# Kernel optimization log

Hardware: AMD Instinct MI355X
Metric: run time of the kernel (lower is better)

Reference implementation:

```python
import jax, jax.numpy as jnp
import numpy as np

NEG_INF = -9e15  # matches the torch source's large-negative mask value
LRELU_SLOPE = 0.2


def setup_inputs() -> dict:
    key = jax.random.key(0)
    k1, k2, k3, k4, k5, k6 = jax.random.split(key, 6)
    N, D_IN, D_OUT = 8192, 512, 256
    h = jax.random.normal(k1, (N, D_IN), dtype=jnp.float32)
    adj = jax.random.randint(k2, (N, N), 0, 2, dtype=jnp.int32)
    # xavier_uniform with gain=1.414 for W [out, in] and a [1, 2*out]
    lim_W = 1.414 * np.sqrt(6.0 / (D_IN + D_OUT))
    lim_a = 1.414 * np.sqrt(6.0 / (2 * D_OUT + 1))
    W_w = jax.random.uniform(k3, (D_OUT, D_IN), minval=-lim_W, maxval=lim_W, dtype=jnp.float32)
    W_b = jax.random.normal(k4, (D_OUT,), dtype=jnp.float32) * 0.01
    a_w = jax.random.uniform(k5, (1, 2 * D_OUT), minval=-lim_a, maxval=lim_a, dtype=jnp.float32)
    a_b = jax.random.normal(k6, (1,), dtype=jnp.float32) * 0.01
    return {"h": h, "adj": adj, "W_w": W_w, "W_b": W_b, "a_w": a_w, "a_b": a_b}


def reference(h, adj, W_w, W_b, a_w, a_b):
    # wh = W(h): [N, d_out]
    wh = h @ W_w.T + W_b
    d_out = wh.shape[-1]
    # a(cat([wh_i, wh_j])) decomposes: a_src . wh_i + a_dst . wh_j + a_b
    # (identical math to the O(N^2 * 2d) repeat/cat in the torch source)
    a_src, a_dst = a_w[0, :d_out], a_w[0, d_out:]
    s_src = wh @ a_src  # [N]
    s_dst = wh @ a_dst  # [N]
    e = jax.nn.leaky_relu(s_src[:, None] + s_dst[None, :] + a_b[0], LRELU_SLOPE)  # [N, N]
    masked = jnp.where(adj > 0, e, jnp.float32(NEG_INF))
    attn = jax.nn.softmax(masked, axis=1)  # softmax over neighbors j
    return attn @ wh  # [N, d_out]
```

## Files before the change

### kernel.cpp

```cpp
#include <hip/hip_runtime.h>

typedef unsigned short ushort_t;
typedef unsigned int uint_t;
typedef __attribute__((ext_vector_type(8))) short short8;
typedef __attribute__((ext_vector_type(4))) float f32x4;
typedef __attribute__((ext_vector_type(4))) int i32x4;
typedef __attribute__((ext_vector_type(4))) uint_t u32x4;
typedef __attribute__((ext_vector_type(4))) ushort_t u16x4;

#define LRELU_SLOPE 0.2f

static __device__ __forceinline__ float bf2f(ushort_t h) {
    uint_t u = ((uint_t)h) << 16;
    return __builtin_bit_cast(float, u);
}
static __device__ __forceinline__ ushort_t f2bf(float f) {
    uint_t u = __builtin_bit_cast(uint_t, f);
    uint_t r = (u + 0x7fffu + ((u >> 16) & 1u)) >> 16;
    return (ushort_t)r;
}
static __device__ __forceinline__ uint4 pack8(float4 a, float4 b) {
    uint4 r;
    r.x = (uint_t)f2bf(a.x) | ((uint_t)f2bf(a.y) << 16);
    r.y = (uint_t)f2bf(a.z) | ((uint_t)f2bf(a.w) << 16);
    r.z = (uint_t)f2bf(b.x) | ((uint_t)f2bf(b.y) << 16);
    r.w = (uint_t)f2bf(b.z) | ((uint_t)f2bf(b.w) << 16);
    return r;
}

__launch_bounds__(256, 2)
__global__ void k1_gemm(const float* __restrict__ h, const float* __restrict__ W,
                        const float* __restrict__ Wb, const float* __restrict__ aw,
                        ushort_t* __restrict__ whT, float* __restrict__ s_src,
                        float* __restrict__ s_dst) {
    __shared__ __align__(16) ushort_t aT[256 * 72];
    __shared__ __align__(16) ushort_t bT[32 * 72];
    __shared__ float redLds[2][4][32];

    const int t = threadIdx.x;
    const int wv = t >> 6, ln = t & 63;
    const int i0 = blockIdx.x * 32;
    const int srow = t >> 3, sch = t & 7;
    const int row0 = ln & 15, kq = ln >> 4;

    f32x4 acc[4][2];
#pragma unroll
    for (int mt = 0; mt < 4; ++mt)
#pragma unroll
        for (int nt = 0; nt < 2; ++nt) acc[mt][nt] = (f32x4){0.f, 0.f, 0.f, 0.f};

    for (int k0 = 0; k0 < 512; k0 += 64) {
        __syncthreads();
#pragma unroll
        for (int r = 0; r < 8; ++r) {
            const float* gp = W + (size_t)(r * 32 + srow) * 512 + k0 + sch * 8;
            float4 x0 = *(const float4*)gp;
            float4 x1 = *(const float4*)(gp + 4);
            *(uint4*)(aT + (r * 32 + srow) * 72 + sch * 8) = pack8(x0, x1);
        }
        {
            const float* gp = h + (size_t)(i0 + srow) * 512 + k0 + sch * 8;
            float4 x0 = *(const float4*)gp;
            float4 x1 = *(const float4*)(gp + 4);
            *(uint4*)(bT + srow * 72 + sch * 8) = pack8(x0, x1);
        }
        __syncthreads();
#pragma unroll
        for (int ks = 0; ks < 2; ++ks) {
            short8 b[2];
#pragma unroll
            for (int nt = 0; nt < 2; ++nt)
                b[nt] = *(const short8*)(bT + (nt * 16 + row0) * 72 + ks * 32 + kq * 8);
#pragma unroll
            for (int mt = 0; mt < 4; ++mt) {
                short8 a = *(const short8*)(aT + (wv * 64 + mt * 16 + row0) * 72 + ks * 32 + kq * 8);
#pragma unroll
                for (int nt = 0; nt < 2; ++nt)
                    acc[mt][nt] = __builtin_amdgcn_mfma_f32_16x16x32_bf16(a, b[nt], acc[mt][nt], 0, 0, 0);
            }
        }
    }

    float psrc[2] = {0.f, 0.f}, pdst[2] = {0.f, 0.f};
#pragma unroll
    for (int mt = 0; mt < 4; ++mt) {
#pragma unroll
        for (int r = 0; r < 4; ++r) {
            const int o = wv * 64 + mt * 16 + (ln >> 4) * 4 + r;
            const float wbv = Wb[o];
            const float as = aw[o];
            const float ad = aw[256 + o];
#pragma unroll
            for (int nt = 0; nt < 2; ++nt) {
                const float v = acc[mt][nt][r] + wbv;
                psrc[nt] += v * as;
                pdst[nt] += v * ad;
                const int i = i0 + nt * 16 + (ln & 15);
                whT[(size_t)o * 8192 + i] = f2bf(v);
            }
        }
    }
#pragma unroll
    for (int off = 16; off < 64; off <<= 1) {
#pragma unroll
        for (int nt = 0; nt < 2; ++nt) {
            psrc[nt] += __shfl_xor(psrc[nt], off, 64);
            pdst[nt] += __shfl_xor(pdst[nt], off, 64);
        }
    }
    if (ln < 16) {
#pragma unroll
        for (int nt = 0; nt < 2; ++nt) {
            redLds[0][wv][nt * 16 + ln] = psrc[nt];
            redLds[1][wv][nt * 16 + ln] = pdst[nt];
        }
    }
    __syncthreads();
    if (t < 32) {
        float s = 0.f;
#pragma unroll
        for (int w = 0; w < 4; ++w) s += redLds[0][w][t];
        s_src[i0 + t] = s;
    } else if (t < 64) {
        float s = 0.f;
#pragma unroll
        for (int w = 0; w < 4; ++w) s += redLds[1][w][t - 32];
        s_dst[i0 + t - 32] = s;
    }
}

__launch_bounds__(512, 4)
__global__ void k2_attn(const int* __restrict__ adj, const ushort_t* __restrict__ whT,
                        const float* __restrict__ s_src, const float* __restrict__ s_dst,
                        const float* __restrict__ ab_p, float* __restrict__ out0,
                        float* __restrict__ out1, float* __restrict__ zp, int jsplit) {
    __shared__ __align__(16) ushort_t wLds[256 * 72];
    __shared__ __align__(16) ushort_t pLds[32 * 72];
    __shared__ float zLds[32];

    const int t = threadIdx.x;
    const int wv = t >> 6, ln = t & 63;
    const int dq = wv & 3, kh = wv >> 2;
    const int split2 = (jsplit == 2);
    const int jb = split2 ? (int)(blockIdx.x & 1) : 0;
    const int ib = split2 ? (int)(blockIdx.x >> 1) : (int)blockIdx.x;
    const int i0 = ib * 32;
    const int jlen = split2 ? 4096 : 8192;
    const int jbase = jb * jlen;
    const int iters = jlen >> 6;
    const int prow = t >> 4, pjc = t & 15;
    const int srow = t >> 3, sch = t & 7;

    const float ab = ab_p[0];
    const float ssrc = s_src[i0 + prow];

    const int* aBase = adj + (size_t)(i0 + prow) * 8192 + jbase + pjc * 4;
    const float* sBase = s_dst + jbase + pjc * 4;
    const ushort_t* wBase = whT + (size_t)srow * 8192 + jbase + sch * 8;
    ushort_t* pDst = pLds + prow * 72 + pjc * 4;

    f32x4 acc[2][4];
#pragma unroll
    for (int mt = 0; mt < 2; ++mt)
#pragma unroll
        for (int nt = 0; nt < 4; ++nt) acc[mt][nt] = (f32x4){0.f, 0.f, 0.f, 0.f};
    float zacc = 0.f;

    i32x4 Av = *(const i32x4*)aBase;
    f32x4 Sv = *(const f32x4*)sBase;
    u32x4 Wv[4];
#pragma unroll
    for (int r = 0; r < 4; ++r) Wv[r] = *(const u32x4*)(wBase + (size_t)r * 64 * 8192);

    for (int it = 0; it < iters; ++it) {
        const int jn = (it < iters - 1) ? (it + 1) * 64 : it * 64;
        i32x4 Ac = Av;
        f32x4 Sc = Sv;
        u32x4 Wc[4];
#pragma unroll
        for (int r = 0; r < 4; ++r) Wc[r] = Wv[r];
        Av = *(const i32x4*)(aBase + jn);
        Sv = *(const f32x4*)(sBase + jn);
#pragma unroll
        for (int r = 0; r < 4; ++r) Wv[r] = *(const u32x4*)(wBase + (size_t)r * 64 * 8192 + jn);

        __syncthreads();
#pragma unroll
        for (int r = 0; r < 4; ++r)
            *(u32x4*)(wLds + (r * 64 + srow) * 72 + sch * 8) = Wc[r];
        {
            u16x4 pv4;
            float z4 = 0.f;
#pragma unroll
            for (int k = 0; k < 4; ++k) {
                float sc = ssrc + Sc[k] + ab;
                sc = sc > 0.f ? sc : LRELU_SLOPE * sc;
                sc = fminf(sc, 60.f);
                float pv = (Ac[k] > 0) ? __expf(sc) : 0.f;
                z4 += pv;
                pv4[k] = f2bf(pv);
            }
            zacc += z4;
            *(u16x4*)pDst = pv4;
        }
        __syncthreads();
        {
            short8 b[4];
#pragma unroll
            for (int nt = 0; nt < 4; ++nt)
                b[nt] = *(const short8*)(wLds + (dq * 64 + nt * 16 + (ln & 15)) * 72 + kh * 32 + (ln >> 4) * 8);
#pragma unroll
            for (int mt = 0; mt < 2; ++mt) {
                short8 a = *(const short8*)(pLds + (mt * 16 + (ln & 15)) * 72 + kh * 32 + (ln >> 4) * 8);
#pragma unroll
                for (int nt = 0; nt < 4; ++nt)
                    acc[mt][nt] = __builtin_amdgcn_mfma_f32_16x16x32_bf16(a, b[nt], acc[mt][nt], 0, 0, 0);
            }
        }
    }

    zacc += __shfl_xor(zacc, 1, 64);
    zacc += __shfl_xor(zacc, 2, 64);
    zacc += __shfl_xor(zacc, 4, 64);
    zacc += __shfl_xor(zacc, 8, 64);
    if (split2) {
        if ((t & 15) == 0) zp[(size_t)jb * 8192 + i0 + prow] = zacc;
    } else {
        if ((t & 15) == 0) zLds[prow] = 1.0f / fmaxf(zacc, 1e-30f);
    }

    __syncthreads();
    float* ex = (float*)wLds;
    if (kh == 1) {
        float* p = ex + (dq * 64 + ln) * 33;
#pragma unroll
        for (int mt = 0; mt < 2; ++mt)
#pragma unroll
            for (int nt = 0; nt < 4; ++nt)
#pragma unroll
                for (int r = 0; r < 4; ++r) p[mt * 16 + nt * 4 + r] = acc[mt][nt][r];
    }
    __syncthreads();
    if (kh == 0) {
        float* outp = (jb == 0) ? out0 : out1;
        const float* p = ex + (dq * 64 + ln) * 33;
#pragma unroll
        for (int mt = 0; mt < 2; ++mt)
#pragma unroll
            for (int nt = 0; nt < 4; ++nt)
#pragma unroll
                for (int r = 0; r < 4; ++r) {
                    const int il = mt * 16 + (ln >> 4) * 4 + r;
                    const int d = dq * 64 + nt * 16 + (ln & 15);
                    const float v = acc[mt][nt][r] + p[mt * 16 + nt * 4 + r];
                    if (split2)
                        outp[(size_t)(i0 + il) * 256 + d] = v;
                    else
                        outp[(size_t)(i0 + il) * 256 + d] = v * zLds[il];
                }
    }
}

__global__ void k3_norm(float* __restrict__ out, const float* __restrict__ part,
                        const float* __restrict__ zp) {
    const int i = blockIdx.x, t = threadIdx.x;
    const float rz = 1.0f / fmaxf(zp[i] + zp[8192 + i], 1e-30f);
    const size_t idx = (size_t)i * 256 + t;
    out[idx] = (out[idx] + part[idx]) * rz;
}

extern "C" void kernel_launch(void* const* d_in, const int* in_sizes, int n_in, void* d_out,
                              int out_size, void* d_ws, size_t ws_size, hipStream_t stream) {
    int order[16];
    for (int i = 0; i < n_in; ++i) order[i] = i;
    for (int a = 0; a < n_in; ++a)
        for (int b = a + 1; b < n_in; ++b)
            if (in_sizes[order[b]] < in_sizes[order[a]]) {
                int tmp = order[a]; order[a] = order[b]; order[b] = tmp;
            }
    const float* ab = (const float*)d_in[order[0]];
    const float* Wb = (const float*)d_in[order[1]];
    const float* aw = (const float*)d_in[order[2]];
    const float* Ww = (const float*)d_in[order[3]];
    const float* h = (const float*)d_in[order[4]];
    const int* adj = (const int*)d_in[order[5]];

    char* ws = (char*)d_ws;
    ushort_t* whT = (ushort_t*)ws;
    float* ssrc = (float*)(ws + 4194304);
    float* sdst = (float*)(ws + 4227072);
    float* part = (float*)(ws + 4259840);
    float* zp = (float*)(ws + 12648448);
    const size_t need = 12713984;
    const int jsplit = (ws_size >= need) ? 2 : 1;

    hipLaunchKernelGGL(k1_gemm, dim3(256), dim3(256), 0, stream, h, Ww, Wb, aw, whT, ssrc, sdst);
    hipLaunchKernelGGL(k2_attn, dim3(256 * jsplit), dim3(512), 0, stream, adj, whT, ssrc, sdst,
                       ab, (float*)d_out, part, zp, jsplit);
    if (jsplit == 2)
        hipLaunchKernelGGL(k3_norm, dim3(8192), dim3(256), 0, stream, (float*)d_out, part, zp);
}
```

Measured before the change: 442.5 us.

## Pre-swizzle wh into MFMA fragment layout and load B operands directly from global

The first kernel now writes wh in a blocked layout that matches the MFMA B-fragment order. The attention kernel can then load B operands straight from global memory into registers, which removes the per-iteration LDS staging of a 256x64 tile. The P tile is double-buffered in LDS, so one of the two barriers per iteration is dropped, and adj is read with nontemporal loads. In exchange, each wave loads its own B fragments from global memory or L2 with no LDS sharing, and the whB write pattern in the first kernel becomes more scattered.

```diff
diff --git a/kernel.cpp b/kernel.cpp
--- a/kernel.cpp
+++ b/kernel.cpp
@@ -10,10 +10,6 @@
 
 #define LRELU_SLOPE 0.2f
 
-static __device__ __forceinline__ float bf2f(ushort_t h) {
-    uint_t u = ((uint_t)h) << 16;
-    return __builtin_bit_cast(float, u);
-}
 static __device__ __forceinline__ ushort_t f2bf(float f) {
     uint_t u = __builtin_bit_cast(uint_t, f);
     uint_t r = (u + 0x7fffu + ((u >> 16) & 1u)) >> 16;
@@ -31,7 +27,7 @@
 __launch_bounds__(256, 2)
 __global__ void k1_gemm(const float* __restrict__ h, const float* __restrict__ W,
                         const float* __restrict__ Wb, const float* __restrict__ aw,
-                        ushort_t* __restrict__ whT, float* __restrict__ s_src,
+                        ushort_t* __restrict__ whB, float* __restrict__ s_src,
                         float* __restrict__ s_dst) {
     __shared__ __align__(16) ushort_t aT[256 * 72];
     __shared__ __align__(16) ushort_t bT[32 * 72];
@@ -96,7 +92,10 @@
                 psrc[nt] += v * as;
                 pdst[nt] += v * ad;
                 const int i = i0 + nt * 16 + (ln & 15);
-                whT[(size_t)o * 8192 + i] = f2bf(v);
+                const int jt = i >> 6;
+                const int khi = (i >> 5) & 1;
+                const int kqi = (i >> 3) & 3;
+                whB[((size_t)(jt * 2 + khi) * 256 + o) * 32 + kqi * 8 + (i & 7)] = f2bf(v);
             }
         }
     }
@@ -130,17 +129,19 @@
 }
 
 __launch_bounds__(512, 4)
-__global__ void k2_attn(const int* __restrict__ adj, const ushort_t* __restrict__ whT,
+__global__ void k2_attn(const int* __restrict__ adj, const ushort_t* __restrict__ whB,
                         const float* __restrict__ s_src, const float* __restrict__ s_dst,
                         const float* __restrict__ ab_p, float* __restrict__ out0,
                         float* __restrict__ out1, float* __restrict__ zp, int jsplit) {
-    __shared__ __align__(16) ushort_t wLds[256 * 72];
-    __shared__ __align__(16) ushort_t pLds[32 * 72];
-    __shared__ float zLds[32];
+    __shared__ __align__(16) char smem[33792 + 128];
+    ushort_t* pbuf = (ushort_t*)smem;
+    float* exch = (float*)smem;
+    float* zLds = (float*)(smem + 33792);
 
     const int t = threadIdx.x;
     const int wv = t >> 6, ln = t & 63;
     const int dq = wv & 3, kh = wv >> 2;
+    const int row0 = ln & 15, kq = ln >> 4;
     const int split2 = (jsplit == 2);
     const int jb = split2 ? (int)(blockIdx.x & 1) : 0;
     const int ib = split2 ? (int)(blockIdx.x >> 1) : (int)blockIdx.x;
@@ -149,15 +150,14 @@
     const int jbase = jb * jlen;
     const int iters = jlen >> 6;
     const int prow = t >> 4, pjc = t & 15;
-    const int srow = t >> 3, sch = t & 7;
 
     const float ab = ab_p[0];
     const float ssrc = s_src[i0 + prow];
 
     const int* aBase = adj + (size_t)(i0 + prow) * 8192 + jbase + pjc * 4;
     const float* sBase = s_dst + jbase + pjc * 4;
-    const ushort_t* wBase = whT + (size_t)srow * 8192 + jbase + sch * 8;
-    ushort_t* pDst = pLds + prow * 72 + pjc * 4;
+    const ushort_t* bBase = whB + ((size_t)(jbase >> 6) * 2 + kh) * 8192
+                            + (dq * 64 + row0) * 32 + kq * 8;
 
     f32x4 acc[2][4];
 #pragma unroll
@@ -166,28 +166,28 @@
         for (int nt = 0; nt < 4; ++nt) acc[mt][nt] = (f32x4){0.f, 0.f, 0.f, 0.f};
     float zacc = 0.f;
 
-    i32x4 Av = *(const i32x4*)aBase;
+    i32x4 Av = __builtin_nontemporal_load((const i32x4*)aBase);
     f32x4 Sv = *(const f32x4*)sBase;
-    u32x4 Wv[4];
-#pragma unroll
-    for (int r = 0; r < 4; ++r) Wv[r] = *(const u32x4*)(wBase + (size_t)r * 64 * 8192);
+    short8 Bv[4];
+#pragma unroll
+    for (int nt = 0; nt < 4; ++nt) Bv[nt] = *(const short8*)(bBase + nt * 512);
 
     for (int it = 0; it < iters; ++it) {
-        const int jn = (it < iters - 1) ? (it + 1) * 64 : it * 64;
+        const int itn = (it < iters - 1) ? it + 1 : it;
+        const int jn = itn * 64;
         i32x4 Ac = Av;
         f32x4 Sc = Sv;
-        u32x4 Wc[4];
-#pragma unroll
-        for (int r = 0; r < 4; ++r) Wc[r] = Wv[r];
-        Av = *(const i32x4*)(aBase + jn);
+        short8 Bc[4];
+#pragma unroll
+        for (int nt = 0; nt < 4; ++nt) Bc[nt] = Bv[nt];
+        Av = __builtin_nontemporal_load((const i32x4*)(aBase + jn));
         Sv = *(const f32x4*)(sBase + jn);
-#pragma unroll
-        for (int r = 0; r < 4; ++r) Wv[r] = *(const u32x4*)(wBase + (size_t)r * 64 * 8192 + jn);
-
-        __syncthreads();
-#pragma unroll
-        for (int r = 0; r < 4; ++r)
-            *(u32x4*)(wLds + (r * 64 + srow) * 72 + sch * 8) = Wc[r];
+        {
+            const ushort_t* bN = bBase + (size_t)itn * 16384;
+#pragma unroll
+            for (int nt = 0; nt < 4; ++nt) Bv[nt] = *(const short8*)(bN + nt * 512);
+        }
+
         {
             u16x4 pv4;
             float z4 = 0.f;
@@ -201,20 +201,17 @@
                 pv4[k] = f2bf(pv);
             }
             zacc += z4;
-            *(u16x4*)pDst = pv4;
+            *(u16x4*)(pbuf + (it & 1) * 2304 + prow * 72 + pjc * 4) = pv4;
         }
         __syncthreads();
         {
-            short8 b[4];
-#pragma unroll
-            for (int nt = 0; nt < 4; ++nt)
-                b[nt] = *(const short8*)(wLds + (dq * 64 + nt * 16 + (ln & 15)) * 72 + kh * 32 + (ln >> 4) * 8);
-#pragma unroll
-            for (int mt = 0; mt < 2; ++mt) {
-                short8 a = *(const short8*)(pLds + (mt * 16 + (ln & 15)) * 72 + kh * 32 + (ln >> 4) * 8);
-#pragma unroll
-                for (int nt = 0; nt < 4; ++nt)
-                    acc[mt][nt] = __builtin_amdgcn_mfma_f32_16x16x32_bf16(a, b[nt], acc[mt][nt], 0, 0, 0);
+            const ushort_t* pc = pbuf + (it & 1) * 2304;
+            short8 a0 = *(const short8*)(pc + row0 * 72 + kh * 32 + kq * 8);
+            short8 a1 = *(const short8*)(pc + (16 + row0) * 72 + kh * 32 + kq * 8);
+#pragma unroll
+            for (int nt = 0; nt < 4; ++nt) {
+                acc[0][nt] = __builtin_amdgcn_mfma_f32_16x16x32_bf16(a0, Bc[nt], acc[0][nt], 0, 0, 0);
+                acc[1][nt] = __builtin_amdgcn_mfma_f32_16x16x32_bf16(a1, Bc[nt], acc[1][nt], 0, 0, 0);
             }
         }
     }
@@ -230,9 +227,8 @@
     }
 
     __syncthreads();
-    float* ex = (float*)wLds;
     if (kh == 1) {
-        float* p = ex + (dq * 64 + ln) * 33;
+        float* p = exch + (dq * 64 + ln) * 33;
 #pragma unroll
         for (int mt = 0; mt < 2; ++mt)
 #pragma unroll
@@ -243,7 +239,7 @@
     __syncthreads();
     if (kh == 0) {
         float* outp = (jb == 0) ? out0 : out1;
-        const float* p = ex + (dq * 64 + ln) * 33;
+        const float* p = exch + (dq * 64 + ln) * 33;
 #pragma unroll
         for (int mt = 0; mt < 2; ++mt)
 #pragma unroll
@@ -286,7 +282,7 @@
     const int* adj = (const int*)d_in[order[5]];
 
     char* ws = (char*)d_ws;
-    ushort_t* whT = (ushort_t*)ws;
+    ushort_t* whB = (ushort_t*)ws;
     float* ssrc = (float*)(ws + 4194304);
     float* sdst = (float*)(ws + 4227072);
     float* part = (float*)(ws + 4259840);
@@ -294,8 +290,8 @@
     const size_t need = 12713984;
     const int jsplit = (ws_size >= need) ? 2 : 1;
 
-    hipLaunchKernelGGL(k1_gemm, dim3(256), dim3(256), 0, stream, h, Ww, Wb, aw, whT, ssrc, sdst);
-    hipLaunchKernelGGL(k2_attn, dim3(256 * jsplit), dim3(512), 0, stream, adj, whT, ssrc, sdst,
+    hipLaunchKernelGGL(k1_gemm, dim3(256), dim3(256), 0, stream, h, Ww, Wb, aw, whB, ssrc, sdst);
+    hipLaunchKernelGGL(k2_attn, dim3(256 * jsplit), dim3(512), 0, stream, adj, whB, ssrc, sdst,
                        ab, (float*)d_out, part, zp, jsplit);
     if (jsplit == 2)
         hipLaunchKernelGGL(k3_norm, dim3(8192), dim3(256), 0, stream, (float*)d_out, part, zp);
```

After: 432.2 us. 2.3% less time.
